# Optimization experiments

Measured on AMD Instinct MI355X. Metric: run time of the kernel, lower is better.

The kernel has to match this reference:

```python
import jax, jax.numpy as jnp
import numpy as np

INPUT_SIZE = 512
HIDDEN_SIZE = 2048
OUTPUT_SIZE = 512
NUM_LAYERS = 4
INNER = INPUT_SIZE + HIDDEN_SIZE  # 2560
BATCH = 4096


def setup_inputs() -> dict:
    key = jax.random.key(0)
    ks = jax.random.split(key, 5)
    scale = 1.0 / np.sqrt(INNER)  # kaiming-uniform-like scale for nn.Linear
    x = jax.random.normal(ks[0], (BATCH, INPUT_SIZE), dtype=jnp.float32)
    h = jax.random.normal(ks[1], (BATCH, HIDDEN_SIZE), dtype=jnp.float32)
    W_layers = jax.random.normal(ks[2], (NUM_LAYERS, INNER, INNER), dtype=jnp.float32) * scale
    b_layers = jnp.zeros((NUM_LAYERS, INNER), dtype=jnp.float32)
    W_i2h = jax.random.normal(ks[3], (HIDDEN_SIZE, INNER), dtype=jnp.float32) * scale
    b_i2h = jnp.zeros((HIDDEN_SIZE,), dtype=jnp.float32)
    W_i2o = jax.random.normal(ks[4], (OUTPUT_SIZE, INNER), dtype=jnp.float32) * scale
    b_i2o = jnp.zeros((OUTPUT_SIZE,), dtype=jnp.float32)
    return {"x": x, "h": h, "W_layers": W_layers, "b_layers": b_layers,
            "W_i2h": W_i2h, "b_i2h": b_i2h, "W_i2o": W_i2o, "b_i2o": b_i2o}


def reference(x, h, W_layers, b_layers, W_i2h, b_i2h, W_i2o, b_i2o):
    # combined: [B, inner]
    combined = jnp.concatenate([x, h], axis=1)
    # stack of square Hebbian linear layers + ReLU (imprint trace writes are
    # state side effects only; they do not affect the forward output)
    for l in range(W_layers.shape[0]):
        combined = jax.nn.relu(jnp.einsum('bi,oi->bo', combined, W_layers[l]) + b_layers[l])
    hidden = jnp.tanh(jnp.einsum('bi,oi->bo', combined, W_i2h) + b_i2h)
    output = jnp.einsum('bi,oi->bo', combined, W_i2o) + b_i2o
    return (output, hidden)
```

## Files before the change

kernel.cpp:

```cpp
#include <hip/hip_runtime.h>
#include <hip/hip_bf16.h>

#define BATCH 4096
#define IN_SZ 512
#define HID_SZ 2048
#define OUT_SZ 512
#define NLAYER 4
#define INNER 2560
#define NKT (INNER / 64)


typedef __attribute__((ext_vector_type(8))) short bf16x8;
typedef __attribute__((ext_vector_type(4))) float f32x4;

__device__ __forceinline__ unsigned short f2bf(float f) {
  unsigned int u = __float_as_uint(f);
  u += 0x7fff + ((u >> 16) & 1);
  return (unsigned short)(u >> 16);
}

__device__ __forceinline__ void gload16(const void* g, void* l) {
  __builtin_amdgcn_global_load_lds(
      (const __attribute__((address_space(1))) unsigned int*)g,
      (__attribute__((address_space(3))) unsigned int*)l,
      16, 0, 0);
}


__global__ void cvt_f32_bf16(const float* __restrict__ in,
                             unsigned short* __restrict__ out, int n4) {
  int i = blockIdx.x * blockDim.x + threadIdx.x;
  const int stride = gridDim.x * blockDim.x;
  for (; i < n4; i += stride) {
    float4 v = *reinterpret_cast<const float4*>(in + (long)i * 4);
    ushort4 o;
    o.x = f2bf(v.x); o.y = f2bf(v.y); o.z = f2bf(v.z); o.w = f2bf(v.w);
    *reinterpret_cast<ushort4*>(out + (long)i * 4) = o;
  }
}

__global__ void build_combined(const float* __restrict__ x,
                               const float* __restrict__ h,
                               unsigned short* __restrict__ out) {
  const int n4 = BATCH * INNER / 4;
  int i = blockIdx.x * blockDim.x + threadIdx.x;
  const int stride = gridDim.x * blockDim.x;
  for (; i < n4; i += stride) {
    int row = i / (INNER / 4);
    int c4 = i - row * (INNER / 4);
    const float* src = (c4 < IN_SZ / 4) ? (x + (long)row * IN_SZ + c4 * 4)
                                        : (h + (long)row * HID_SZ + (c4 - IN_SZ / 4) * 4);
    float4 v = *reinterpret_cast<const float4*>(src);
    ushort4 o;
    o.x = f2bf(v.x); o.y = f2bf(v.y); o.z = f2bf(v.z); o.w = f2bf(v.w);
    *reinterpret_cast<ushort4*>(out + (long)i * 4) = o;
  }
}


#define STAGE_U(kt, u, buf) do {                                              \
  if ((u) < 2) {                                                              \
    const int base_ = (u) * 64 + w * 8;                                       \
    gload16(A + (long)(row0 + base_ + srow) * INNER + (kt) * 64 + srcsw,      \
            (void*)(&lds[buf][base_ * 64]));                                  \
  } else {                                                                    \
    const int base_ = ((u) - 2) * 64 + w * 8;                                 \
    gload16(B + (long)(col0 + base_ + srow) * INNER + (kt) * 64 + srcsw,      \
            (void*)(&lds[buf][8192 + base_ * 64]));                           \
  } } while (0)

#define LOAD_AF2(mh, buf) do {                                                \
  const unsigned short* Ar_ = &lds[buf][0];                                   \
  _Pragma("unroll")                                                           \
  for (int m_ = 0; m_ < 2; ++m_) {                                            \
    int r_ = wr * 64 + (mh) * 32 + m_ * 16 + fr;                              \
    af2[m_][0] = *(const bf16x8*)(Ar_ + r_ * 64 + csw0);                      \
    af2[m_][1] = *(const bf16x8*)(Ar_ + r_ * 64 + csw1);                      \
  } } while (0)

#define LOAD_BQA(buf) do {                                                    \
  const unsigned short* Br_ = &lds[buf][8192];                                \
  _Pragma("unroll")                                                           \
  for (int n_ = 0; n_ < 3; ++n_) {                                            \
    int r_ = wcn * 80 + n_ * 16 + fr;                                         \
    bqA[n_][0] = *(const bf16x8*)(Br_ + r_ * 64 + csw0);                      \
    bqA[n_][1] = *(const bf16x8*)(Br_ + r_ * 64 + csw1);                      \
  } } while (0)

#define LOAD_BQB(buf) do {                                                    \
  const unsigned short* Br_ = &lds[buf][8192];                                \
  _Pragma("unroll")                                                           \
  for (int n_ = 0; n_ < 2; ++n_) {                                            \
    int r_ = wcn * 80 + (3 + n_) * 16 + fr;                                   \
    bqB[n_][0] = *(const bf16x8*)(Br_ + r_ * 64 + csw0);                      \
    bqB[n_][1] = *(const bf16x8*)(Br_ + r_ * 64 + csw1);                      \
  } } while (0)

#define MF_A(mh) do {                                                         \
  __builtin_amdgcn_s_setprio(1);                                              \
  _Pragma("unroll")                                                           \
  for (int m_ = 0; m_ < 2; ++m_)                                              \
    _Pragma("unroll")                                                         \
    for (int n_ = 0; n_ < 3; ++n_) {                                          \
      acc[(mh) * 2 + m_][n_] = __builtin_amdgcn_mfma_f32_16x16x32_bf16(       \
          af2[m_][0], bqA[n_][0], acc[(mh) * 2 + m_][n_], 0, 0, 0);           \
      acc[(mh) * 2 + m_][n_] = __builtin_amdgcn_mfma_f32_16x16x32_bf16(       \
          af2[m_][1], bqA[n_][1], acc[(mh) * 2 + m_][n_], 0, 0, 0);           \
    }                                                                         \
  __builtin_amdgcn_s_setprio(0);                                              \
} while (0)

#define MF_B(mh) do {                                                         \
  __builtin_amdgcn_s_setprio(1);                                              \
  _Pragma("unroll")                                                           \
  for (int m_ = 0; m_ < 2; ++m_)                                              \
    _Pragma("unroll")                                                         \
    for (int n_ = 0; n_ < 2; ++n_) {                                          \
      acc[(mh) * 2 + m_][3 + n_] = __builtin_amdgcn_mfma_f32_16x16x32_bf16(   \
          af2[m_][0], bqB[n_][0], acc[(mh) * 2 + m_][3 + n_], 0, 0, 0);       \
      acc[(mh) * 2 + m_][3 + n_] = __builtin_amdgcn_mfma_f32_16x16x32_bf16(   \
          af2[m_][1], bqB[n_][1], acc[(mh) * 2 + m_][3 + n_], 0, 0, 0);       \
    }                                                                         \
  __builtin_amdgcn_s_setprio(0);                                              \
} while (0)

#define SYNC_MFMA() do {                                                      \
  __builtin_amdgcn_s_barrier();                                               \
  asm volatile("s_waitcnt lgkmcnt(0)" ::: "memory");                          \
  __builtin_amdgcn_sched_barrier(0);                                          \
} while (0)

template <int MODE>
__global__ __launch_bounds__(512, 2)
void gemm8(const unsigned short* __restrict__ A, const unsigned short* __restrict__ B,
           const float* __restrict__ bias0, const float* __restrict__ bias1,
           void* __restrict__ C) {
  __shared__ unsigned short lds[2][28672];

  const int tid = threadIdx.x;
  const int w = tid >> 6;
  const int lane = tid & 63;

  const int flat = blockIdx.x;
  const int nb = flat & 7;
  const int mb = flat >> 3;
  const int row0 = mb * 128, col0 = nb * 320;
  const int wr = w >> 2, wcn = w & 3;

  const int srow = lane >> 3;
  const int srcsw = ((((lane & 7) << 4) ^ ((lane >> 3) << 4)) >> 1);

  const int fr = lane & 15;
  const int csw0 = ((((lane >> 4) << 4)) ^ ((lane & 7) << 4)) >> 1;
  const int csw1 = ((64 + ((lane >> 4) << 4)) ^ ((lane & 7) << 4)) >> 1;

  f32x4 acc[4][5] = {};
  bf16x8 af2[2][2], bqA[3][2], bqB[2][2];

  STAGE_U(0, 0, 0); STAGE_U(0, 1, 0); STAGE_U(0, 2, 0); STAGE_U(0, 3, 0);
  STAGE_U(0, 4, 0); STAGE_U(0, 5, 0); STAGE_U(0, 6, 0);
  STAGE_U(1, 2, 1); STAGE_U(1, 3, 1); STAGE_U(1, 4, 1);
  asm volatile("s_waitcnt vmcnt(3)" ::: "memory");
  __builtin_amdgcn_s_barrier();
  __builtin_amdgcn_sched_barrier(0);

  for (int T = 0; T < NKT; ++T) {
    const int d = T & 1;
    const int kt1 = (T + 1 < NKT) ? T + 1 : NKT - 1;
    const int kt2 = (T + 2 < NKT) ? T + 2 : NKT - 1;

    LOAD_AF2(0, d);
    LOAD_BQA(d);
    STAGE_U(kt1, 5, d ^ 1); STAGE_U(kt1, 6, d ^ 1);
    asm volatile("s_waitcnt lgkmcnt(6)" ::: "memory");
    SYNC_MFMA();
    MF_A(0);
    __builtin_amdgcn_s_barrier();

    LOAD_BQB(d);
    STAGE_U(kt1, 0, d ^ 1); STAGE_U(kt1, 1, d ^ 1);
    SYNC_MFMA();
    MF_B(0);
    __builtin_amdgcn_s_barrier();

    LOAD_AF2(1, d);
    STAGE_U(kt2, 2, d); STAGE_U(kt2, 3, d);
    SYNC_MFMA();
    MF_B(1);
    __builtin_amdgcn_s_barrier();

    STAGE_U(kt2, 4, d);
    asm volatile("s_waitcnt vmcnt(3)" ::: "memory");
    __builtin_amdgcn_s_barrier();
    __builtin_amdgcn_sched_barrier(0);
    MF_A(1);
    __builtin_amdgcn_s_barrier();
  }
  asm volatile("s_waitcnt vmcnt(0)" ::: "memory");

  const int erow = row0 + wr * 64 + ((lane >> 4) << 2);
  const int ecol = col0 + wcn * 80 + fr;
  if (MODE == 0) {
    unsigned short* Co = (unsigned short*)C;
#pragma unroll
    for (int n = 0; n < 5; ++n) {
      const int col = ecol + n * 16;
      const float bv = bias0[col];
#pragma unroll
      for (int m = 0; m < 4; ++m) {
        const int row = erow + m * 16;
#pragma unroll
        for (int j = 0; j < 4; ++j) {
          float v = acc[m][n][j] + bv;
          v = fmaxf(v, 0.0f);
          Co[(long)(row + j) * INNER + col] = f2bf(v);
        }
      }
    }
  } else {
    float* outO = (float*)C;
    float* outH = (float*)C + (long)BATCH * OUT_SZ;
#pragma unroll
    for (int n = 0; n < 5; ++n) {
      const int col = ecol + n * 16;
      if (col < OUT_SZ) {
        const float bv = bias0[col];
#pragma unroll
        for (int m = 0; m < 4; ++m) {
          const int row = erow + m * 16;
#pragma unroll
          for (int j = 0; j < 4; ++j)
            outO[(long)(row + j) * OUT_SZ + col] = acc[m][n][j] + bv;
        }
      } else {
        const int hc = col - OUT_SZ;
        const float bv = bias1[hc];
#pragma unroll
        for (int m = 0; m < 4; ++m) {
          const int row = erow + m * 16;
#pragma unroll
          for (int j = 0; j < 4; ++j)
            outH[(long)(row + j) * HID_SZ + hc] = tanhf(acc[m][n][j] + bv);
        }
      }
    }
  }
}


extern "C" void kernel_launch(void* const* d_in, const int* in_sizes, int n_in,
                              void* d_out, int out_size, void* d_ws, size_t ws_size,
                              hipStream_t stream) {
  const float* x   = (const float*)d_in[0];
  const float* h   = (const float*)d_in[1];
  const float* Wl  = (const float*)d_in[2];
  const float* bl  = (const float*)d_in[3];
  const float* Wih = (const float*)d_in[4];
  const float* bih = (const float*)d_in[5];
  const float* Wio = (const float*)d_in[6];
  const float* bio = (const float*)d_in[7];

  unsigned short* ws   = (unsigned short*)d_ws;
  unsigned short* Wlb  = ws;
  unsigned short* Whb  = Wlb + (long)NLAYER * INNER * INNER;
  unsigned short* act0 = Whb + (long)INNER * INNER;
  unsigned short* act1 = act0 + (long)BATCH * INNER;

  cvt_f32_bf16<<<2048, 256, 0, stream>>>(Wl,  Wlb, NLAYER * INNER * INNER / 4);
  cvt_f32_bf16<<<256,  256, 0, stream>>>(Wio, Whb, OUT_SZ * INNER / 4);
  cvt_f32_bf16<<<1024, 256, 0, stream>>>(Wih, Whb + (long)OUT_SZ * INNER, HID_SZ * INNER / 4);
  build_combined<<<2048, 256, 0, stream>>>(x, h, act0);

  unsigned short* a_in = act0;
  unsigned short* a_out = act1;
  for (int l = 0; l < NLAYER; ++l) {
    gemm8<0><<<256, 512, 0, stream>>>(a_in, Wlb + (long)l * INNER * INNER,
                                      bl + (long)l * INNER, nullptr, a_out);
    unsigned short* t = a_in; a_in = a_out; a_out = t;
  }

  gemm8<1><<<256, 512, 0, stream>>>(a_in, Whb, bio, bih, d_out);
}
```

Baseline: 344.9 us.

## Prefetch next tile's LDS fragments into double-buffered registers during MFMA phases

Restructures the k-loop into a two-tile unrolled body with ping-pong register sets for the A and B fragments. The next tile's first A/Bq fragments are loaded from LDS at the end of the current tile, and the later fragments are loaded one phase ahead, so LDS reads overlap MFMA work and the waits relax to lgkmcnt(4). This hides LDS read latency at the cost of more VGPRs, which could cause spills or hurt occupancy under launch_bounds(512,2).

```diff
diff --git a/kernel.cpp b/kernel.cpp
--- a/kernel.cpp
+++ b/kernel.cpp
@@ -69,65 +69,103 @@
             (void*)(&lds[buf][8192 + base_ * 64]));                           \
   } } while (0)
 
-#define LOAD_AF2(mh, buf) do {                                                \
-  const unsigned short* Ar_ = &lds[buf][0];                                   \
-  _Pragma("unroll")                                                           \
-  for (int m_ = 0; m_ < 2; ++m_) {                                            \
-    int r_ = wr * 64 + (mh) * 32 + m_ * 16 + fr;                              \
-    af2[m_][0] = *(const bf16x8*)(Ar_ + r_ * 64 + csw0);                      \
-    af2[m_][1] = *(const bf16x8*)(Ar_ + r_ * 64 + csw1);                      \
-  } } while (0)
-
-#define LOAD_BQA(buf) do {                                                    \
-  const unsigned short* Br_ = &lds[buf][8192];                                \
-  _Pragma("unroll")                                                           \
-  for (int n_ = 0; n_ < 3; ++n_) {                                            \
-    int r_ = wcn * 80 + n_ * 16 + fr;                                         \
-    bqA[n_][0] = *(const bf16x8*)(Br_ + r_ * 64 + csw0);                      \
-    bqA[n_][1] = *(const bf16x8*)(Br_ + r_ * 64 + csw1);                      \
-  } } while (0)
-
-#define LOAD_BQB(buf) do {                                                    \
-  const unsigned short* Br_ = &lds[buf][8192];                                \
-  _Pragma("unroll")                                                           \
-  for (int n_ = 0; n_ < 2; ++n_) {                                            \
-    int r_ = wcn * 80 + (3 + n_) * 16 + fr;                                   \
-    bqB[n_][0] = *(const bf16x8*)(Br_ + r_ * 64 + csw0);                      \
-    bqB[n_][1] = *(const bf16x8*)(Br_ + r_ * 64 + csw1);                      \
-  } } while (0)
-
-#define MF_A(mh) do {                                                         \
+#define LOAD_AF(dst, mh, buf) do {                                           \
+  const unsigned short* Ar_ = &lds[buf][0];                                  \
+  _Pragma("unroll")                                                          \
+  for (int m_ = 0; m_ < 2; ++m_) {                                           \
+    int r_ = wr * 64 + (mh) * 32 + m_ * 16 + fr;                             \
+    dst[m_][0] = *(const bf16x8*)(Ar_ + r_ * 64 + csw0);                     \
+    dst[m_][1] = *(const bf16x8*)(Ar_ + r_ * 64 + csw1);                     \
+  } } while (0)
+
+#define LOAD_BQA(dst, buf) do {                                              \
+  const unsigned short* Br_ = &lds[buf][8192];                               \
+  _Pragma("unroll")                                                          \
+  for (int n_ = 0; n_ < 3; ++n_) {                                           \
+    int r_ = wcn * 80 + n_ * 16 + fr;                                        \
+    dst[n_][0] = *(const bf16x8*)(Br_ + r_ * 64 + csw0);                     \
+    dst[n_][1] = *(const bf16x8*)(Br_ + r_ * 64 + csw1);                     \
+  } } while (0)
+
+#define LOAD_BQB(dst, buf) do {                                              \
+  const unsigned short* Br_ = &lds[buf][8192];                               \
+  _Pragma("unroll")                                                          \
+  for (int n_ = 0; n_ < 2; ++n_) {                                           \
+    int r_ = wcn * 80 + (3 + n_) * 16 + fr;                                  \
+    dst[n_][0] = *(const bf16x8*)(Br_ + r_ * 64 + csw0);                     \
+    dst[n_][1] = *(const bf16x8*)(Br_ + r_ * 64 + csw1);                     \
+  } } while (0)
+
+#define MF_A(af, bq, mh) do {                                                 \
   __builtin_amdgcn_s_setprio(1);                                              \
   _Pragma("unroll")                                                           \
   for (int m_ = 0; m_ < 2; ++m_)                                              \
     _Pragma("unroll")                                                         \
     for (int n_ = 0; n_ < 3; ++n_) {                                          \
       acc[(mh) * 2 + m_][n_] = __builtin_amdgcn_mfma_f32_16x16x32_bf16(       \
-          af2[m_][0], bqA[n_][0], acc[(mh) * 2 + m_][n_], 0, 0, 0);           \
+          af[m_][0], bq[n_][0], acc[(mh) * 2 + m_][n_], 0, 0, 0);             \
       acc[(mh) * 2 + m_][n_] = __builtin_amdgcn_mfma_f32_16x16x32_bf16(       \
-          af2[m_][1], bqA[n_][1], acc[(mh) * 2 + m_][n_], 0, 0, 0);           \
+          af[m_][1], bq[n_][1], acc[(mh) * 2 + m_][n_], 0, 0, 0);             \
     }                                                                         \
   __builtin_amdgcn_s_setprio(0);                                              \
 } while (0)
 
-#define MF_B(mh) do {                                                         \
+#define MF_B(af, bq, mh) do {                                                 \
   __builtin_amdgcn_s_setprio(1);                                              \
   _Pragma("unroll")                                                           \
   for (int m_ = 0; m_ < 2; ++m_)                                              \
     _Pragma("unroll")                                                         \
     for (int n_ = 0; n_ < 2; ++n_) {                                          \
       acc[(mh) * 2 + m_][3 + n_] = __builtin_amdgcn_mfma_f32_16x16x32_bf16(   \
-          af2[m_][0], bqB[n_][0], acc[(mh) * 2 + m_][3 + n_], 0, 0, 0);       \
+          af[m_][0], bq[n_][0], acc[(mh) * 2 + m_][3 + n_], 0, 0, 0);         \
       acc[(mh) * 2 + m_][3 + n_] = __builtin_amdgcn_mfma_f32_16x16x32_bf16(   \
-          af2[m_][1], bqB[n_][1], acc[(mh) * 2 + m_][3 + n_], 0, 0, 0);       \
+          af[m_][1], bq[n_][1], acc[(mh) * 2 + m_][3 + n_], 0, 0, 0);         \
     }                                                                         \
   __builtin_amdgcn_s_setprio(0);                                              \
 } while (0)
 
-#define SYNC_MFMA() do {                                                      \
-  __builtin_amdgcn_s_barrier();                                               \
-  asm volatile("s_waitcnt lgkmcnt(0)" ::: "memory");                          \
-  __builtin_amdgcn_sched_barrier(0);                                          \
+#define SB() __builtin_amdgcn_sched_barrier(0)
+
+#define TILE_BODY(d, AC, QC, AN, QN) do {                                     \
+  const int T = T2 + (d);                                                     \
+  const int kt1 = (T + 1 < NKT) ? T + 1 : NKT - 1;                            \
+  const int kt2 = (T + 2 < NKT) ? T + 2 : NKT - 1;                            \
+            \
+  LOAD_BQB(bqB, d);                                                           \
+  STAGE_U(kt1, 5, (d) ^ 1); STAGE_U(kt1, 6, (d) ^ 1);                         \
+  SB();                                                                       \
+  __builtin_amdgcn_s_barrier();                                               \
+  asm volatile("s_waitcnt lgkmcnt(4)" ::: "memory");          \
+  SB();                                                                       \
+  MF_A(AC, QC, 0);                                                            \
+  __builtin_amdgcn_s_barrier();                                               \
+           \
+  LOAD_AF(afB, 1, d);                                                         \
+  STAGE_U(kt1, 0, (d) ^ 1); STAGE_U(kt1, 1, (d) ^ 1);                         \
+  SB();                                                                       \
+  __builtin_amdgcn_s_barrier();                                               \
+  asm volatile("s_waitcnt lgkmcnt(4)" ::: "memory");            \
+  SB();                                                                       \
+  MF_B(AC, bqB, 0);                                                           \
+  __builtin_amdgcn_s_barrier();                                               \
+                          \
+  STAGE_U(kt2, 2, d); STAGE_U(kt2, 3, d);                                     \
+  SB();                                                                       \
+  __builtin_amdgcn_s_barrier();                                               \
+  asm volatile("s_waitcnt lgkmcnt(0)" ::: "memory");            \
+  SB();                                                                       \
+  MF_B(afB, bqB, 1);                                                          \
+  __builtin_amdgcn_s_barrier();                                               \
+       \
+  STAGE_U(kt2, 4, d);                                                         \
+  asm volatile("s_waitcnt vmcnt(3)" ::: "memory");      \
+  __builtin_amdgcn_s_barrier();                                               \
+  SB();                                                                       \
+  LOAD_AF(AN, 0, (d) ^ 1);                                                    \
+  LOAD_BQA(QN, (d) ^ 1);                                                      \
+  SB();                           \
+  MF_A(afB, QC, 1);                                                           \
+  __builtin_amdgcn_s_barrier();                                               \
 } while (0)
 
 template <int MODE>
@@ -155,46 +193,22 @@
   const int csw1 = ((64 + ((lane >> 4) << 4)) ^ ((lane & 7) << 4)) >> 1;
 
   f32x4 acc[4][5] = {};
-  bf16x8 af2[2][2], bqA[3][2], bqB[2][2];
+  bf16x8 afA0[2][2], afA1[2][2], afB[2][2];
+  bf16x8 bqA0[3][2], bqA1[3][2], bqB[2][2];
 
   STAGE_U(0, 0, 0); STAGE_U(0, 1, 0); STAGE_U(0, 2, 0); STAGE_U(0, 3, 0);
   STAGE_U(0, 4, 0); STAGE_U(0, 5, 0); STAGE_U(0, 6, 0);
   STAGE_U(1, 2, 1); STAGE_U(1, 3, 1); STAGE_U(1, 4, 1);
   asm volatile("s_waitcnt vmcnt(3)" ::: "memory");
   __builtin_amdgcn_s_barrier();
-  __builtin_amdgcn_sched_barrier(0);
-
-  for (int T = 0; T < NKT; ++T) {
-    const int d = T & 1;
-    const int kt1 = (T + 1 < NKT) ? T + 1 : NKT - 1;
-    const int kt2 = (T + 2 < NKT) ? T + 2 : NKT - 1;
-
-    LOAD_AF2(0, d);
-    LOAD_BQA(d);
-    STAGE_U(kt1, 5, d ^ 1); STAGE_U(kt1, 6, d ^ 1);
-    asm volatile("s_waitcnt lgkmcnt(6)" ::: "memory");
-    SYNC_MFMA();
-    MF_A(0);
-    __builtin_amdgcn_s_barrier();
-
-    LOAD_BQB(d);
-    STAGE_U(kt1, 0, d ^ 1); STAGE_U(kt1, 1, d ^ 1);
-    SYNC_MFMA();
-    MF_B(0);
-    __builtin_amdgcn_s_barrier();
-
-    LOAD_AF2(1, d);
-    STAGE_U(kt2, 2, d); STAGE_U(kt2, 3, d);
-    SYNC_MFMA();
-    MF_B(1);
-    __builtin_amdgcn_s_barrier();
-
-    STAGE_U(kt2, 4, d);
-    asm volatile("s_waitcnt vmcnt(3)" ::: "memory");
-    __builtin_amdgcn_s_barrier();
-    __builtin_amdgcn_sched_barrier(0);
-    MF_A(1);
-    __builtin_amdgcn_s_barrier();
+  SB();
+  LOAD_AF(afA0, 0, 0);
+  LOAD_BQA(bqA0, 0);
+  SB();
+
+  for (int T2 = 0; T2 < NKT; T2 += 2) {
+    TILE_BODY(0, afA0, bqA0, afA1, bqA1);
+    TILE_BODY(1, afA1, bqA1, afA0, bqA0);
   }
   asm volatile("s_waitcnt vmcnt(0)" ::: "memory");
 
```

Measured after the change: 310.7 us. -9.9%, faster.
